# Kernel optimization log

Measured on AMD Instinct MI355X. Metric: run time of the kernel, lower is better.

Reference implementation:

```python
import jax, jax.numpy as jnp
import numpy as np

D_MODEL = 768
N_HEAD = 12
HEAD_DIM = D_MODEL // N_HEAD
SCALE = HEAD_DIM ** -0.5
B, T = 8, 1024
NEG_INF = -1e9


def setup_inputs() -> dict:
    key = jax.random.key(0)
    ks = jax.random.split(key, 4)
    x = jax.random.normal(ks[0], (B, T, D_MODEL), dtype=jnp.float32)
    W_attn = jax.random.normal(ks[1], (D_MODEL, 3 * D_MODEL), dtype=jnp.float32) * 0.02
    b_attn = jnp.zeros((3 * D_MODEL,), dtype=jnp.float32)
    W_proj = jax.random.normal(ks[2], (D_MODEL, D_MODEL), dtype=jnp.float32) * 0.02
    b_proj = jnp.zeros((D_MODEL,), dtype=jnp.float32)
    return {"x": x, "W_attn": W_attn, "b_attn": b_attn, "W_proj": W_proj, "b_proj": b_proj}


def reference(x, W_attn, b_attn, W_proj, b_proj):
    Bn, Tn, C = x.shape
    # fused QKV projection: [B,T,3C]
    qkv = jnp.einsum('btc,cd->btd', x, W_attn) + b_attn
    q, k, v = jnp.split(qkv, 3, axis=-1)
    # [B, H, T, hd]
    def heads(t):
        return t.reshape(Bn, Tn, N_HEAD, HEAD_DIM).transpose(0, 2, 1, 3)
    q, k, v = heads(q), heads(k), heads(v)
    # scaled dot-product scores [B,H,T,T]
    att = jnp.einsum('bhqd,bhkd->bhqk', q, k) * SCALE
    # causal mask: mask[i,j]=1 where j>i (upper triangle, excluded)
    causal = jnp.tril(jnp.ones((Tn, Tn), dtype=bool))
    att = jnp.where(causal[None, None, :, :], att, NEG_INF)
    att = jax.nn.softmax(att, axis=-1)
    # weighted value sum -> merge heads
    y = jnp.einsum('bhqk,bhkd->bhqd', att, v)
    y = y.transpose(0, 2, 1, 3).reshape(Bn, Tn, C)
    # output projection
    return jnp.einsum('btc,cd->btd', y, W_proj) + b_proj
```

## Files before the change

kernel.cpp:

```cpp
#include <hip/hip_runtime.h>
#include <hip/hip_bf16.h>

#define T_SEQ 1024
#define NBATCH 8
#define NHEAD 12
#define HD 64
#define CDIM 768
#define C3 2304
#define ATT_SCALE 0.125f

typedef __attribute__((ext_vector_type(8))) __bf16 bf16x8;
typedef __attribute__((ext_vector_type(4))) __bf16 bf16x4;
typedef __attribute__((ext_vector_type(2))) __bf16 bf16x2;
typedef __attribute__((ext_vector_type(4))) float  f32x4;

__device__ __forceinline__ f32x4 mfma_bf16(bf16x8 a, bf16x8 b, f32x4 c) {
    return __builtin_amdgcn_mfma_f32_16x16x32_bf16(a, b, c, 0, 0, 0);
}

__device__ __forceinline__ void gload16(const void* g, void* l) {
    __builtin_amdgcn_global_load_lds(
        (const __attribute__((address_space(1))) unsigned int*)g,
        (__attribute__((address_space(3))) unsigned int*)l, 16, 0, 0);
}

#define WAIT_VM(N) do { asm volatile("s_waitcnt vmcnt(" #N ")" ::: "memory"); \
                        __builtin_amdgcn_sched_barrier(0); } while (0)
#define WAIT_LGKM0 do { asm volatile("s_waitcnt lgkmcnt(0)" ::: "memory"); \
                        __builtin_amdgcn_sched_barrier(0); } while (0)

__global__ __launch_bounds__(256) void cvt_f32_bf16(const float* __restrict__ in,
                                                    __bf16* __restrict__ out, int n4) {
    int i = blockIdx.x * 256 + threadIdx.x;
    if (i < n4) {
        float4 v = ((const float4*)in)[i];
        bf16x4 o = { (__bf16)v.x, (__bf16)v.y, (__bf16)v.z, (__bf16)v.w };
        ((bf16x4*)out)[i] = o;
    }
}

__global__ __launch_bounds__(256) void transpose_cvt(const float* __restrict__ W,
                                                     __bf16* __restrict__ Wt,
                                                     int R, int C) {
    __shared__ float tile[32][33];
    const int c0 = blockIdx.x * 32, r0 = blockIdx.y * 32;
    const int tc = threadIdx.x & 31, tr = threadIdx.x >> 5;
#pragma unroll
    for (int i = 0; i < 4; ++i)
        tile[tr + i * 8][tc] = W[(size_t)(r0 + tr + i * 8) * C + c0 + tc];
    __syncthreads();
#pragma unroll
    for (int i = 0; i < 4; ++i)
        Wt[(size_t)(c0 + tr + i * 8) * R + r0 + tc] = (__bf16)tile[tc][tr + i * 8];
}

template<int OUT_BF16>
__global__ __launch_bounds__(256) void gemm_bt(const __bf16* __restrict__ A,
                                               const __bf16* __restrict__ Bt,
                                               const float* __restrict__ bias,
                                               void* __restrict__ Cout,
                                               int M, int N, int K, int nbx) {
    __shared__ __align__(16) __bf16 sA[3][128 * 32];
    __shared__ __align__(16) __bf16 sB[3][128 * 32];
    const int t = threadIdx.x, l = t & 63, w = t >> 6;
    const int lr = l & 15, lk = l >> 4;
    const int wr = w >> 1, wc = w & 1;
    const int q = gridDim.x >> 3;
    const int swz = (blockIdx.x & 7) * q + (blockIdx.x >> 3);
    const int m0 = (swz / nbx) * 128, n0 = (swz % nbx) * 128;

    const int r_st = t >> 2;
    const int c_st = t & 3;
    const int sw_st = (r_st & 3) ^ ((r_st >> 2) & 3);
    const int g_off = (c_st ^ sw_st) << 3;
    const int sw_rd = (lr & 3) ^ ((lr >> 2) & 3);

    f32x4 acc[4][4];
#pragma unroll
    for (int m = 0; m < 4; ++m)
#pragma unroll
        for (int n = 0; n < 4; ++n) acc[m][n] = f32x4{0.f, 0.f, 0.f, 0.f};

    const int nk = K >> 5;

#pragma unroll
    for (int s = 0; s < 3; ++s) {
        const int k0 = s << 5;
#pragma unroll
        for (int i = 0; i < 2; ++i) {
            int r = i * 64 + r_st;
            gload16(A + (size_t)(m0 + r) * K + k0 + g_off,
                    (char*)&sA[s][0] + (i * 256 + w * 64) * 16);
            gload16(Bt + (size_t)(n0 + r) * K + k0 + g_off,
                    (char*)&sB[s][0] + (i * 256 + w * 64) * 16);
        }
    }

    int cur = 0;
    for (int kt = 0; kt < nk; ++kt) {
        if (kt + 2 < nk)      WAIT_VM(8);
        else if (kt + 1 < nk) WAIT_VM(4);
        else                  WAIT_VM(0);
        __builtin_amdgcn_s_barrier();

        bf16x8 af[4], bg[4];
#pragma unroll
        for (int m = 0; m < 4; ++m)
            af[m] = *(const bf16x8*)(&sA[cur][(wr * 64 + m * 16 + lr) * 32 + ((lk ^ sw_rd) << 3)]);
#pragma unroll
        for (int n = 0; n < 4; ++n)
            bg[n] = *(const bf16x8*)(&sB[cur][(wc * 64 + n * 16 + lr) * 32 + ((lk ^ sw_rd) << 3)]);
        WAIT_LGKM0;
        __builtin_amdgcn_s_barrier();

        if (kt + 3 < nk) {
            const int k0 = (kt + 3) << 5;
#pragma unroll
            for (int i = 0; i < 2; ++i) {
                int r = i * 64 + r_st;
                gload16(A + (size_t)(m0 + r) * K + k0 + g_off,
                        (char*)&sA[cur][0] + (i * 256 + w * 64) * 16);
                gload16(Bt + (size_t)(n0 + r) * K + k0 + g_off,
                        (char*)&sB[cur][0] + (i * 256 + w * 64) * 16);
            }
        }

#pragma unroll
        for (int m = 0; m < 4; ++m)
#pragma unroll
            for (int n = 0; n < 4; ++n)
                acc[m][n] = mfma_bf16(af[m], bg[n], acc[m][n]);

        cur = (cur == 2) ? 0 : cur + 1;
    }

#pragma unroll
    for (int n = 0; n < 4; ++n) {
        int col = n0 + wc * 64 + n * 16 + lr;
        float bv = bias[col];
#pragma unroll
        for (int m = 0; m < 4; ++m) {
            int row0 = m0 + wr * 64 + m * 16 + lk * 4;
#pragma unroll
            for (int j = 0; j < 4; ++j) {
                float v = acc[m][n][j] + bv;
                if (OUT_BF16)
                    ((__bf16*)Cout)[(size_t)(row0 + j) * N + col] = (__bf16)v;
                else
                    ((float*)Cout)[(size_t)(row0 + j) * N + col] = v;
            }
        }
    }
}

__global__ __launch_bounds__(256, 2) void attn_fwd(const __bf16* __restrict__ qkv,
                                                   __bf16* __restrict__ y) {
    const int tid = threadIdx.x, l = tid & 63, w = tid >> 6;
    const int lr = l & 15, lk = l >> 4;
    const int r7 = lr & 7;
    const int bid = blockIdx.x;
    const int pr = bid / 96;
    const int hb = bid % 96;
    const int h = hb % NHEAD;
    const int b = hb / NHEAD;

    __shared__ __align__(16) __bf16 sK[2][64][64];
    __shared__ __align__(16) __bf16 sV[2][64][64];
    __shared__ __align__(16) __bf16 sP[4][16][72];

    const size_t baseQ = (size_t)b * T_SEQ * C3 + h * HD;
    const __bf16* Kp = qkv + baseQ + CDIM;
    const __bf16* Vp = qkv + baseQ + 2 * CDIM;

    const int vk0 = tid >> 3;
    const int vc = (tid & 7) << 3;
    const int vg = tid & 7;
    const int krow = tid >> 3;
    const int kchunk = (tid & 7) ^ ((tid >> 3) & 7);

#pragma unroll 1
    for (int job = 0; job < 2; ++job) {
        const int qt = (job == 0) ? pr : 15 - pr;
        const int q0 = qt * 64;
        const int nt = qt + 1;
        const int q_abs = q0 + w * 16 + lr;

        const size_t rowQ = baseQ + (size_t)(q0 + w * 16 + lr) * C3;
        bf16x8 qa0 = *(const bf16x8*)(qkv + rowQ + lk * 8);
        bf16x8 qa1 = *(const bf16x8*)(qkv + rowQ + 32 + lk * 8);

        f32x4 acc[4];
#pragma unroll
        for (int fd = 0; fd < 4; ++fd) acc[fd] = f32x4{0.f, 0.f, 0.f, 0.f};
        float mrun = -1e30f, lrun = 0.f;

        bf16x8 vreg[2];
#pragma unroll
        for (int i = 0; i < 2; ++i)
            vreg[i] = *(const bf16x8*)(Vp + (size_t)(i * 32 + vk0) * C3 + vc);
#pragma unroll
        for (int i = 0; i < 2; ++i)
            gload16(Kp + (size_t)(i * 32 + krow) * C3 + kchunk * 8,
                    (char*)&sK[0][0][0] + (i * 256 + w * 64) * 16);
#pragma unroll
        for (int i = 0; i < 2; ++i) {
            int key = i * 32 + vk0;
#pragma unroll
            for (int e = 0; e < 8; ++e)
                sV[0][vc + e][key ^ ((e ^ vg) << 3)] = vreg[i][e];
        }
        __syncthreads();

#pragma unroll 1
        for (int t = 0; t < nt; ++t) {
            const int kv0 = t * 64;
            const int cur = t & 1, nxt = cur ^ 1;
            const bool pre = (t + 1 < nt);
            if (pre) {
                const int kvp = kv0 + 64;
#pragma unroll
                for (int i = 0; i < 2; ++i)
                    vreg[i] = *(const bf16x8*)(Vp + (size_t)(kvp + i * 32 + vk0) * C3 + vc);
#pragma unroll
                for (int i = 0; i < 2; ++i)
                    gload16(Kp + (size_t)(kvp + i * 32 + krow) * C3 + kchunk * 8,
                            (char*)&sK[nxt][0][0] + (i * 256 + w * 64) * 16);
            }
            f32x4 s[4];
#pragma unroll
            for (int fc = 0; fc < 4; ++fc) {
                const __bf16* kr = &sK[cur][fc * 16 + lr][0];
                bf16x8 k0 = *(const bf16x8*)(kr + ((lk ^ r7) << 3));
                bf16x8 k1 = *(const bf16x8*)(kr + (((4 + lk) ^ r7) << 3));
                f32x4 z = f32x4{0.f, 0.f, 0.f, 0.f};
                z = mfma_bf16(k0, qa0, z);
                z = mfma_bf16(k1, qa1, z);
                s[fc] = z;
            }
            float ps[4][4];
#pragma unroll
            for (int fc = 0; fc < 4; ++fc)
#pragma unroll
                for (int j = 0; j < 4; ++j) {
                    int key = kv0 + fc * 16 + lk * 4 + j;
                    ps[fc][j] = (key <= q_abs) ? s[fc][j] * ATT_SCALE : -1e30f;
                }
            float mt = -1e30f;
#pragma unroll
            for (int fc = 0; fc < 4; ++fc)
#pragma unroll
                for (int j = 0; j < 4; ++j) mt = fmaxf(mt, ps[fc][j]);
            mt = fmaxf(mt, __shfl_xor(mt, 16, 64));
            mt = fmaxf(mt, __shfl_xor(mt, 32, 64));
            const float mn = fmaxf(mrun, mt);
            const float corr = __expf(mrun - mn);
            mrun = mn;
            float rs = 0.f;
#pragma unroll
            for (int fc = 0; fc < 4; ++fc)
#pragma unroll
                for (int j = 0; j < 4; ++j) {
                    float p = __expf(ps[fc][j] - mn);
                    ps[fc][j] = p;
                    rs += p;
                }
            rs += __shfl_xor(rs, 16, 64);
            rs += __shfl_xor(rs, 32, 64);
            lrun = lrun * corr + rs;
            float cj[4];
#pragma unroll
            for (int j = 0; j < 4; ++j) cj[j] = __shfl(corr, lk * 4 + j, 64);
#pragma unroll
            for (int fd = 0; fd < 4; ++fd)
#pragma unroll
                for (int j = 0; j < 4; ++j) acc[fd][j] *= cj[j];
#pragma unroll
            for (int fc = 0; fc < 4; ++fc)
#pragma unroll
                for (int jp = 0; jp < 2; ++jp) {
                    bf16x2 pk = { (__bf16)ps[fc][jp * 2], (__bf16)ps[fc][jp * 2 + 1] };
                    *(bf16x2*)&sP[w][lr][fc * 16 + lk * 4 + jp * 2] = pk;
                }
#pragma unroll
            for (int ks = 0; ks < 2; ++ks) {
                bf16x8 pa = *(const bf16x8*)&sP[w][lr][ks * 32 + lk * 8];
#pragma unroll
                for (int fd = 0; fd < 4; ++fd) {
                    int d = fd * 16 + lr;
                    int sw = ((d & 7) ^ ((d >> 3) & 7)) << 3;
                    bf16x8 vb = *(const bf16x8*)&sV[cur][d][(ks * 32 + lk * 8) ^ sw];
                    acc[fd] = mfma_bf16(pa, vb, acc[fd]);
                }
            }
            if (pre) {
#pragma unroll
                for (int i = 0; i < 2; ++i) {
                    int key = i * 32 + vk0;
#pragma unroll
                    for (int e = 0; e < 8; ++e)
                        sV[nxt][vc + e][key ^ ((e ^ vg) << 3)] = vreg[i][e];
                }
            }
            __syncthreads();
        }

        float linv[4];
#pragma unroll
        for (int j = 0; j < 4; ++j) linv[j] = 1.f / __shfl(lrun, lk * 4 + j, 64);
        const size_t yrow0 = (size_t)(b * T_SEQ + q0 + w * 16 + lk * 4);
#pragma unroll
        for (int fd = 0; fd < 4; ++fd) {
            int col = h * HD + fd * 16 + lr;
#pragma unroll
            for (int j = 0; j < 4; ++j)
                y[(yrow0 + j) * CDIM + col] = (__bf16)(acc[fd][j] * linv[j]);
        }
    }
}

extern "C" void kernel_launch(void* const* d_in, const int* in_sizes, int n_in,
                              void* d_out, int out_size, void* d_ws, size_t ws_size,
                              hipStream_t stream) {
    const float* x      = (const float*)d_in[0];
    const float* W_attn = (const float*)d_in[1];
    const float* b_attn = (const float*)d_in[2];
    const float* W_proj = (const float*)d_in[3];
    const float* b_proj = (const float*)d_in[4];

    __bf16* xb  = (__bf16*)d_ws;
    __bf16* Wat = xb  + (size_t)8192 * 768;
    __bf16* Wpt = Wat + (size_t)2304 * 768;
    __bf16* qkv = Wpt + (size_t)768 * 768;
    __bf16* yb  = qkv + (size_t)8192 * 2304;

    cvt_f32_bf16<<<6144, 256, 0, stream>>>(x, xb, (8192 * 768) / 4);
    transpose_cvt<<<dim3(72, 24), 256, 0, stream>>>(W_attn, Wat, 768, 2304);
    transpose_cvt<<<dim3(24, 24), 256, 0, stream>>>(W_proj, Wpt, 768, 768);

    gemm_bt<1><<<18 * 64, 256, 0, stream>>>(xb, Wat, b_attn, (void*)qkv, 8192, 2304, 768, 18);
    attn_fwd<<<NBATCH * NHEAD * 8, 256, 0, stream>>>(qkv, yb);
    gemm_bt<0><<<6 * 64, 256, 0, stream>>>(yb, Wpt, b_proj, d_out, 8192, 768, 768, 6);
}
```

Before: 118.0 us.

## Add 256x128 tiled 512-thread QKV GEMM and MFMA priority hints in attention

Replaces the QKV projection GEMM with a new kernel that uses 512-thread blocks computing 256x128 output tiles, so each B tile loaded into LDS is reused across twice as many rows. It keeps a three-stage global-to-LDS prefetch. The attention kernel raises wave priority with s_setprio around its MFMA sections, and the wait macros no longer include sched_barrier, which gives the compiler more freedom to schedule around them. The larger block raises LDS use per block and halves the grid size, which may reduce occupancy and tail balance.

```diff
diff --git a/kernel.cpp b/kernel.cpp
--- a/kernel.cpp
+++ b/kernel.cpp
@@ -24,10 +24,8 @@
         (__attribute__((address_space(3))) unsigned int*)l, 16, 0, 0);
 }
 
-#define WAIT_VM(N) do { asm volatile("s_waitcnt vmcnt(" #N ")" ::: "memory"); \
-                        __builtin_amdgcn_sched_barrier(0); } while (0)
-#define WAIT_LGKM0 do { asm volatile("s_waitcnt lgkmcnt(0)" ::: "memory"); \
-                        __builtin_amdgcn_sched_barrier(0); } while (0)
+#define WAIT_VM(N)  asm volatile("s_waitcnt vmcnt(" #N ")" ::: "memory")
+#define WAIT_LGKM0  asm volatile("s_waitcnt lgkmcnt(0)" ::: "memory")
 
 __global__ __launch_bounds__(256) void cvt_f32_bf16(const float* __restrict__ in,
                                                     __bf16* __restrict__ out, int n4) {
@@ -52,6 +50,95 @@
 #pragma unroll
     for (int i = 0; i < 4; ++i)
         Wt[(size_t)(c0 + tr + i * 8) * R + r0 + tc] = (__bf16)tile[tc][tr + i * 8];
+}
+
+__global__ __launch_bounds__(512) void gemm_qkv(const __bf16* __restrict__ A,
+                                                const __bf16* __restrict__ Bt,
+                                                const float* __restrict__ bias,
+                                                __bf16* __restrict__ Cout,
+                                                int M, int N, int K, int nbx) {
+    __shared__ __align__(16) __bf16 sA[3][256 * 32];
+    __shared__ __align__(16) __bf16 sB[3][128 * 32];
+    const int t = threadIdx.x, l = t & 63, w = t >> 6;
+    const int lr = l & 15, lk = l >> 4;
+    const int wr = w >> 1, wc = w & 1;
+    const int q = gridDim.x >> 3;
+    const int swz = (blockIdx.x & 7) * q + (blockIdx.x >> 3);
+    const int m0 = (swz / nbx) * 256, n0 = (swz % nbx) * 128;
+
+    const int sw_st = ((t >> 2) & 3) ^ ((t >> 4) & 3);
+    const int g_off = ((t & 3) ^ sw_st) << 3;
+    const int sw_rd = (lr & 3) ^ ((lr >> 2) & 3);
+
+    f32x4 acc[4][4];
+#pragma unroll
+    for (int m = 0; m < 4; ++m)
+#pragma unroll
+        for (int n = 0; n < 4; ++n) acc[m][n] = f32x4{0.f, 0.f, 0.f, 0.f};
+
+    const int nk = K >> 5;
+    const int rA = t >> 2;
+    const int rB = t >> 2;
+
+#pragma unroll
+    for (int s = 0; s < 3; ++s) {
+        const int k0 = s << 5;
+#pragma unroll
+        for (int i = 0; i < 2; ++i)
+            gload16(A + (size_t)(m0 + i * 128 + rA) * K + k0 + g_off,
+                    (char*)&sA[s][0] + (i * 512 + w * 64) * 16);
+        gload16(Bt + (size_t)(n0 + rB) * K + k0 + g_off,
+                (char*)&sB[s][0] + (w * 64) * 16);
+    }
+
+    int cur = 0;
+    for (int kt = 0; kt < nk; ++kt) {
+        if (kt + 2 < nk)      WAIT_VM(6);
+        else if (kt + 1 < nk) WAIT_VM(3);
+        else                  WAIT_VM(0);
+        __builtin_amdgcn_s_barrier();
+
+        bf16x8 af[4], bg[4];
+#pragma unroll
+        for (int m = 0; m < 4; ++m)
+            af[m] = *(const bf16x8*)(&sA[cur][(wr * 64 + m * 16 + lr) * 32 + ((lk ^ sw_rd) << 3)]);
+#pragma unroll
+        for (int n = 0; n < 4; ++n)
+            bg[n] = *(const bf16x8*)(&sB[cur][(wc * 64 + n * 16 + lr) * 32 + ((lk ^ sw_rd) << 3)]);
+        WAIT_LGKM0;
+        __builtin_amdgcn_s_barrier();
+
+        if (kt + 3 < nk) {
+            const int k0 = (kt + 3) << 5;
+#pragma unroll
+            for (int i = 0; i < 2; ++i)
+                gload16(A + (size_t)(m0 + i * 128 + rA) * K + k0 + g_off,
+                        (char*)&sA[cur][0] + (i * 512 + w * 64) * 16);
+            gload16(Bt + (size_t)(n0 + rB) * K + k0 + g_off,
+                    (char*)&sB[cur][0] + (w * 64) * 16);
+        }
+
+#pragma unroll
+        for (int m = 0; m < 4; ++m)
+#pragma unroll
+            for (int n = 0; n < 4; ++n)
+                acc[m][n] = mfma_bf16(af[m], bg[n], acc[m][n]);
+
+        cur = (cur == 2) ? 0 : cur + 1;
+    }
+
+#pragma unroll
+    for (int n = 0; n < 4; ++n) {
+        int col = n0 + wc * 64 + n * 16 + lr;
+        float bv = bias[col];
+#pragma unroll
+        for (int m = 0; m < 4; ++m) {
+            int row0 = m0 + wr * 64 + m * 16 + lk * 4;
+#pragma unroll
+            for (int j = 0; j < 4; ++j)
+                Cout[(size_t)(row0 + j) * N + col] = (__bf16)(acc[m][n][j] + bv);
+        }
+    }
 }
 
 template<int OUT_BF16>
@@ -69,19 +156,18 @@
     const int swz = (blockIdx.x & 7) * q + (blockIdx.x >> 3);
     const int m0 = (swz / nbx) * 128, n0 = (swz % nbx) * 128;
 
+    const int sw_st = ((t >> 2) & 3) ^ ((t >> 4) & 3);
+    const int g_off = ((t & 3) ^ sw_st) << 3;
+    const int sw_rd = (lr & 3) ^ ((lr >> 2) & 3);
+
+    f32x4 acc[4][4];
+#pragma unroll
+    for (int m = 0; m < 4; ++m)
+#pragma unroll
+        for (int n = 0; n < 4; ++n) acc[m][n] = f32x4{0.f, 0.f, 0.f, 0.f};
+
+    const int nk = K >> 5;
     const int r_st = t >> 2;
-    const int c_st = t & 3;
-    const int sw_st = (r_st & 3) ^ ((r_st >> 2) & 3);
-    const int g_off = (c_st ^ sw_st) << 3;
-    const int sw_rd = (lr & 3) ^ ((lr >> 2) & 3);
-
-    f32x4 acc[4][4];
-#pragma unroll
-    for (int m = 0; m < 4; ++m)
-#pragma unroll
-        for (int n = 0; n < 4; ++n) acc[m][n] = f32x4{0.f, 0.f, 0.f, 0.f};
-
-    const int nk = K >> 5;
 
 #pragma unroll
     for (int s = 0; s < 3; ++s) {
@@ -227,6 +313,7 @@
                             (char*)&sK[nxt][0][0] + (i * 256 + w * 64) * 16);
             }
             f32x4 s[4];
+            __builtin_amdgcn_s_setprio(1);
 #pragma unroll
             for (int fc = 0; fc < 4; ++fc) {
                 const __bf16* kr = &sK[cur][fc * 16 + lr][0];
@@ -237,6 +324,7 @@
                 z = mfma_bf16(k1, qa1, z);
                 s[fc] = z;
             }
+            __builtin_amdgcn_s_setprio(0);
             float ps[4][4];
 #pragma unroll
             for (int fc = 0; fc < 4; ++fc)
@@ -281,6 +369,7 @@
                     bf16x2 pk = { (__bf16)ps[fc][jp * 2], (__bf16)ps[fc][jp * 2 + 1] };
                     *(bf16x2*)&sP[w][lr][fc * 16 + lk * 4 + jp * 2] = pk;
                 }
+            __builtin_amdgcn_s_setprio(1);
 #pragma unroll
             for (int ks = 0; ks < 2; ++ks) {
                 bf16x8 pa = *(const bf16x8*)&sP[w][lr][ks * 32 + lk * 8];
@@ -292,6 +381,7 @@
                     acc[fd] = mfma_bf16(pa, vb, acc[fd]);
                 }
             }
+            __builtin_amdgcn_s_setprio(0);
             if (pre) {
 #pragma unroll
                 for (int i = 0; i < 2; ++i) {
@@ -337,7 +427,7 @@
     transpose_cvt<<<dim3(72, 24), 256, 0, stream>>>(W_attn, Wat, 768, 2304);
     transpose_cvt<<<dim3(24, 24), 256, 0, stream>>>(W_proj, Wpt, 768, 768);
 
-    gemm_bt<1><<<18 * 64, 256, 0, stream>>>(xb, Wat, b_attn, (void*)qkv, 8192, 2304, 768, 18);
+    gemm_qkv<<<32 * 18, 512, 0, stream>>>(xb, Wat, b_attn, qkv, 8192, 2304, 768, 18);
     attn_fwd<<<NBATCH * NHEAD * 8, 256, 0, stream>>>(qkv, yb);
     gemm_bt<0><<<6 * 64, 256, 0, stream>>>(yb, Wpt, b_proj, d_out, 8192, 768, 768, 6);
 }
```

After: 122.6 us. 3.9% more time.

## Switch GEMM to 32x32x16 MFMA tiles and add priority hints in attention

Applied to the files above, without the earlier changes.

The QKV and output GEMMs now use the 32x32x16 bf16 MFMA instead of 16x16x32, with a 2x2 grid of 32x32 accumulators per wave and matching fragment loads and epilogue indexing. The MFMAs are moved to run before the second barrier, and the sched_barrier fences are removed from the wait macros so the compiler can overlap work more freely. The attention kernel wraps its two MFMA phases in s_setprio to favour matrix issue over other waves. This trades fewer, larger matrix instructions for a different register layout and a risk of compiler reordering around the hand-written waits.

```diff
diff --git a/kernel.cpp b/kernel.cpp
--- a/kernel.cpp
+++ b/kernel.cpp
@@ -13,9 +13,13 @@
 typedef __attribute__((ext_vector_type(4))) __bf16 bf16x4;
 typedef __attribute__((ext_vector_type(2))) __bf16 bf16x2;
 typedef __attribute__((ext_vector_type(4))) float  f32x4;
+typedef __attribute__((ext_vector_type(16))) float f32x16;
 
 __device__ __forceinline__ f32x4 mfma_bf16(bf16x8 a, bf16x8 b, f32x4 c) {
     return __builtin_amdgcn_mfma_f32_16x16x32_bf16(a, b, c, 0, 0, 0);
+}
+__device__ __forceinline__ f32x16 mfma32(bf16x8 a, bf16x8 b, f32x16 c) {
+    return __builtin_amdgcn_mfma_f32_32x32x16_bf16(a, b, c, 0, 0, 0);
 }
 
 __device__ __forceinline__ void gload16(const void* g, void* l) {
@@ -24,10 +28,8 @@
         (__attribute__((address_space(3))) unsigned int*)l, 16, 0, 0);
 }
 
-#define WAIT_VM(N) do { asm volatile("s_waitcnt vmcnt(" #N ")" ::: "memory"); \
-                        __builtin_amdgcn_sched_barrier(0); } while (0)
-#define WAIT_LGKM0 do { asm volatile("s_waitcnt lgkmcnt(0)" ::: "memory"); \
-                        __builtin_amdgcn_sched_barrier(0); } while (0)
+#define WAIT_VM(N)  asm volatile("s_waitcnt vmcnt(" #N ")" ::: "memory")
+#define WAIT_LGKM0  asm volatile("s_waitcnt lgkmcnt(0)" ::: "memory")
 
 __global__ __launch_bounds__(256) void cvt_f32_bf16(const float* __restrict__ in,
                                                     __bf16* __restrict__ out, int n4) {
@@ -63,23 +65,24 @@
     __shared__ __align__(16) __bf16 sA[3][128 * 32];
     __shared__ __align__(16) __bf16 sB[3][128 * 32];
     const int t = threadIdx.x, l = t & 63, w = t >> 6;
-    const int lr = l & 15, lk = l >> 4;
+    const int l31 = l & 31, lh = l >> 5;
     const int wr = w >> 1, wc = w & 1;
     const int q = gridDim.x >> 3;
     const int swz = (blockIdx.x & 7) * q + (blockIdx.x >> 3);
     const int m0 = (swz / nbx) * 128, n0 = (swz % nbx) * 128;
 
     const int r_st = t >> 2;
-    const int c_st = t & 3;
     const int sw_st = (r_st & 3) ^ ((r_st >> 2) & 3);
-    const int g_off = (c_st ^ sw_st) << 3;
-    const int sw_rd = (lr & 3) ^ ((lr >> 2) & 3);
-
-    f32x4 acc[4][4];
-#pragma unroll
-    for (int m = 0; m < 4; ++m)
-#pragma unroll
-        for (int n = 0; n < 4; ++n) acc[m][n] = f32x4{0.f, 0.f, 0.f, 0.f};
+    const int g_off = ((t & 3) ^ sw_st) << 3;
+    const int sw_rd = (l31 & 3) ^ ((l31 >> 2) & 3);
+
+    f32x16 acc[2][2];
+#pragma unroll
+    for (int m = 0; m < 2; ++m)
+#pragma unroll
+        for (int n = 0; n < 2; ++n)
+#pragma unroll
+            for (int r = 0; r < 16; ++r) acc[m][n][r] = 0.f;
 
     const int nk = K >> 5;
 
@@ -103,13 +106,28 @@
         else                  WAIT_VM(0);
         __builtin_amdgcn_s_barrier();
 
-        bf16x8 af[4], bg[4];
-#pragma unroll
-        for (int m = 0; m < 4; ++m)
-            af[m] = *(const bf16x8*)(&sA[cur][(wr * 64 + m * 16 + lr) * 32 + ((lk ^ sw_rd) << 3)]);
-#pragma unroll
-        for (int n = 0; n < 4; ++n)
-            bg[n] = *(const bf16x8*)(&sB[cur][(wc * 64 + n * 16 + lr) * 32 + ((lk ^ sw_rd) << 3)]);
+        bf16x8 af[2][2], bg[2][2];
+#pragma unroll
+        for (int m = 0; m < 2; ++m)
+#pragma unroll
+            for (int ks = 0; ks < 2; ++ks)
+                af[m][ks] = *(const bf16x8*)(&sA[cur][(wr * 64 + m * 32 + l31) * 32
+                                                      + ((((ks << 1) | lh) ^ sw_rd) << 3)]);
+#pragma unroll
+        for (int n = 0; n < 2; ++n)
+#pragma unroll
+            for (int ks = 0; ks < 2; ++ks)
+                bg[n][ks] = *(const bf16x8*)(&sB[cur][(wc * 64 + n * 32 + l31) * 32
+                                                      + ((((ks << 1) | lh) ^ sw_rd) << 3)]);
+
+#pragma unroll
+        for (int ks = 0; ks < 2; ++ks)
+#pragma unroll
+            for (int m = 0; m < 2; ++m)
+#pragma unroll
+                for (int n = 0; n < 2; ++n)
+                    acc[m][n] = mfma32(af[m][ks], bg[n][ks], acc[m][n]);
+
         WAIT_LGKM0;
         __builtin_amdgcn_s_barrier();
 
@@ -124,30 +142,24 @@
                         (char*)&sB[cur][0] + (i * 256 + w * 64) * 16);
             }
         }
-
-#pragma unroll
-        for (int m = 0; m < 4; ++m)
-#pragma unroll
-            for (int n = 0; n < 4; ++n)
-                acc[m][n] = mfma_bf16(af[m], bg[n], acc[m][n]);
-
         cur = (cur == 2) ? 0 : cur + 1;
     }
 
 #pragma unroll
-    for (int n = 0; n < 4; ++n) {
-        int col = n0 + wc * 64 + n * 16 + lr;
+    for (int n = 0; n < 2; ++n) {
+        int col = n0 + wc * 64 + n * 32 + l31;
         float bv = bias[col];
 #pragma unroll
-        for (int m = 0; m < 4; ++m) {
-            int row0 = m0 + wr * 64 + m * 16 + lk * 4;
-#pragma unroll
-            for (int j = 0; j < 4; ++j) {
-                float v = acc[m][n][j] + bv;
+        for (int m = 0; m < 2; ++m) {
+            int rbase = m0 + wr * 64 + m * 32 + 4 * lh;
+#pragma unroll
+            for (int r = 0; r < 16; ++r) {
+                int row = rbase + (r & 3) + 8 * (r >> 2);
+                float v = acc[m][n][r] + bv;
                 if (OUT_BF16)
-                    ((__bf16*)Cout)[(size_t)(row0 + j) * N + col] = (__bf16)v;
+                    ((__bf16*)Cout)[(size_t)row * N + col] = (__bf16)v;
                 else
-                    ((float*)Cout)[(size_t)(row0 + j) * N + col] = v;
+                    ((float*)Cout)[(size_t)row * N + col] = v;
             }
         }
     }
@@ -227,6 +239,7 @@
                             (char*)&sK[nxt][0][0] + (i * 256 + w * 64) * 16);
             }
             f32x4 s[4];
+            __builtin_amdgcn_s_setprio(1);
 #pragma unroll
             for (int fc = 0; fc < 4; ++fc) {
                 const __bf16* kr = &sK[cur][fc * 16 + lr][0];
@@ -237,6 +250,7 @@
                 z = mfma_bf16(k1, qa1, z);
                 s[fc] = z;
             }
+            __builtin_amdgcn_s_setprio(0);
             float ps[4][4];
 #pragma unroll
             for (int fc = 0; fc < 4; ++fc)
@@ -281,6 +295,7 @@
                     bf16x2 pk = { (__bf16)ps[fc][jp * 2], (__bf16)ps[fc][jp * 2 + 1] };
                     *(bf16x2*)&sP[w][lr][fc * 16 + lk * 4 + jp * 2] = pk;
                 }
+            __builtin_amdgcn_s_setprio(1);
 #pragma unroll
             for (int ks = 0; ks < 2; ++ks) {
                 bf16x8 pa = *(const bf16x8*)&sP[w][lr][ks * 32 + lk * 8];
@@ -292,6 +307,7 @@
                     acc[fd] = mfma_bf16(pa, vb, acc[fd]);
                 }
             }
+            __builtin_amdgcn_s_setprio(0);
             if (pre) {
 #pragma unroll
                 for (int i = 0; i < 2; ++i) {
```

Measured after the change: 118.9 us. About the same (+0.7%).
